# Performance work log

Hardware: AMD Instinct MI355X
Metric: run time of the kernel (lower is better)

Reference implementation:

```python
import jax, jax.numpy as jnp
import numpy as np

IMG_SIZES = [56, 28, 14, 7]


def setup_inputs() -> dict:
    key = jax.random.key(0)
    k0, k1, k2, k3, kp = jax.random.split(key, 5)
    return {
        "feat0": jax.random.normal(k0, (8, 64, 56, 56), dtype=jnp.float32),
        "feat1": jax.random.normal(k1, (8, 128, 28, 28), dtype=jnp.float32),
        "feat2": jax.random.normal(k2, (8, 256, 14, 14), dtype=jnp.float32),
        "feat3": jax.random.normal(k3, (8, 512, 7, 7), dtype=jnp.float32),
        "pts": jax.random.normal(kp, (131072, 3), dtype=jnp.float32),
        "batch": 3,
    }


def _project(feat, h, w, size):
    # feat: [C, size, size]; h, w: [N] float in [0, 223]
    x = h / (224.0 / size)
    y = w / (224.0 / size)
    x1 = jnp.floor(x).astype(jnp.int32)
    x2 = jnp.minimum(jnp.ceil(x).astype(jnp.int32), size - 1)
    y1 = jnp.floor(y).astype(jnp.int32)
    y2 = jnp.minimum(jnp.ceil(y).astype(jnp.int32), size - 1)
    # NOTE: original casts x,y to long BEFORE computing weights (truncation),
    # so weights are integer 0/1 -- reproduced faithfully.
    xl = x.astype(jnp.int32)
    yl = y.astype(jnp.int32)
    g = lambda xi, yi: feat[:, xi, yi].T  # [N, C] gather
    w11 = ((x2 - xl) * (y2 - yl)).astype(feat.dtype)[:, None]
    w12 = ((x2 - xl) * (yl - y1)).astype(feat.dtype)[:, None]
    w21 = ((xl - x1) * (y2 - yl)).astype(feat.dtype)[:, None]
    w22 = ((xl - x1) * (yl - y1)).astype(feat.dtype)[:, None]
    return w11 * g(x1, y1) + w21 * g(x2, y1) + w12 * g(x1, y2) + w22 * g(x2, y2)


def reference(feat0, feat1, feat2, feat3, pts, batch):
    h = 248.0 * (pts[:, 1] / pts[:, 2]) + 111.5
    w = 248.0 * (pts[:, 0] / (-pts[:, 2])) + 111.5
    h = jnp.clip(h, 0.0, 223.0)
    w = jnp.clip(w, 0.0, 223.0)
    feats = [feat0[batch], feat1[batch], feat2[batch], feat3[batch]]
    outs = [_project(f, h, w, s) for f, s in zip(feats, IMG_SIZES)]
    return jnp.concatenate(outs, axis=1)  # [N, 960]
```

## Files before the change

### kernel.cpp

```cpp
#include <hip/hip_runtime.h>
#include <hip/hip_bf16.h>

#define NPTS 131072
#define FT_TOTAL 376320

typedef float f32x4 __attribute__((ext_vector_type(4)));

__global__ __launch_bounds__(256) void k_indices(
    const float* __restrict__ pts,
    int4* __restrict__ idx4)
{
    int n = blockIdx.x * 256 + threadIdx.x;
    if (n >= NPTS) return;
    float px = pts[3 * n + 0];
    float py = pts[3 * n + 1];
    float pz = pts[3 * n + 2];
    float qh = __fdiv_rn(py, pz);
    float qw = __fdiv_rn(px, -pz);
    float h = __fadd_rn(__fmul_rn(248.0f, qh), 111.5f);
    float w = __fadd_rn(__fmul_rn(248.0f, qw), 111.5f);
    h = fminf(fmaxf(h, 0.0f), 223.0f);
    w = fminf(fmaxf(w, 0.0f), 223.0f);

    const float scl[4] = {0.25f, 0.125f, 0.0625f, 0.03125f};
    const int   S[4]   = {56, 28, 14, 7};
    int r[4];
#pragma unroll
    for (int s = 0; s < 4; ++s) {
        float x = h * scl[s];
        float y = w * scl[s];
        int x1 = (int)floorf(x);
        int x2 = min((int)ceilf(x), S[s] - 1);
        int y1 = (int)floorf(y);
        int y2 = min((int)ceilf(y), S[s] - 1);
        int bit = (x2 - x1) * (y2 - y1);
        r[s] = bit ? (x1 * S[s] + y1) : -1;
    }
    idx4[n] = make_int4(r[0], r[1], r[2], r[3]);
}

__global__ __launch_bounds__(256) void k_transpose(
    const float* __restrict__ f0,
    const float* __restrict__ f1,
    const float* __restrict__ f2,
    const float* __restrict__ f3,
    const int* __restrict__ batch,
    float* __restrict__ ft)
{
    int d = blockIdx.x * 256 + threadIdx.x;
    if (d >= FT_TOTAL) return;
    int b = *batch;
    const float* src;
    int local, c, p, hw;
    if (d < 200704) {
        local = d;          c = local & 63;  p = local >> 6; hw = 3136;
        src = f0 + (size_t)b * 64 * 3136;
    } else if (d < 301056) {
        local = d - 200704; c = local & 127; p = local >> 7; hw = 784;
        src = f1 + (size_t)b * 128 * 784;
    } else if (d < 351232) {
        local = d - 301056; c = local & 255; p = local >> 8; hw = 196;
        src = f2 + (size_t)b * 256 * 196;
    } else {
        local = d - 351232; c = local & 511; p = local >> 9; hw = 49;
        src = f3 + (size_t)b * 512 * 49;
    }
    ft[d] = src[c * hw + p];
}

__global__ __launch_bounds__(256) void k_gather(
    const int* __restrict__ idx,
    const float* __restrict__ ft,
    float* __restrict__ out)
{
    int gid = blockIdx.x * 256 + threadIdx.x;
    int n = gid / 240;
    int j = gid - n * 240;

    int s, C, toff, cb;
    if (j < 16)       { s = 0; C = 64;  toff = 0;      cb = j * 4; }
    else if (j < 48)  { s = 1; C = 128; toff = 200704; cb = (j - 16) * 4; }
    else if (j < 112) { s = 2; C = 256; toff = 301056; cb = (j - 48) * 4; }
    else              { s = 3; C = 512; toff = 351232; cb = (j - 112) * 4; }

    int id = idx[n * 4 + s];
    f32x4 v = (f32x4)(0.0f);
    if (id >= 0) {
        v = *(const f32x4*)(ft + toff + id * C + cb);
    }
    f32x4* dst = (f32x4*)(out + (size_t)n * 960 + j * 4);
    __builtin_nontemporal_store(v, dst);
}

extern "C" void kernel_launch(void* const* d_in, const int* in_sizes, int n_in,
                              void* d_out, int out_size, void* d_ws, size_t ws_size,
                              hipStream_t stream) {
    const float* f0  = (const float*)d_in[0];
    const float* f1  = (const float*)d_in[1];
    const float* f2  = (const float*)d_in[2];
    const float* f3  = (const float*)d_in[3];
    const float* pts = (const float*)d_in[4];
    const int* batch = (const int*)d_in[5];

    int4* idx4 = (int4*)d_ws;
    float* ft = (float*)((char*)d_ws + (size_t)NPTS * 16);
    float* out = (float*)d_out;

    k_indices<<<NPTS / 256, 256, 0, stream>>>(pts, idx4);
    k_transpose<<<(FT_TOTAL + 255) / 256, 256, 0, stream>>>(f0, f1, f2, f3, batch, ft);
    k_gather<<<122880, 256, 0, stream>>>((const int*)idx4, ft, out);
}
```

Baseline: 485.9 us.

## Fuse index and transpose kernels; gather one point per wavefront

Merges the index-computation and feature-transpose kernels into one launch that splits work by block range, removing a kernel launch and its serialization. The gather kernel now gives each 64-lane wavefront one point: it loads the four indices once as an int4 and loops over the 240 float4 output chunks, instead of doing a per-thread divide by 240 and a scalar index load. Some lanes are idle in the last loop iteration (240 of 256 slots used), and each thread carries more work.

```diff
diff --git a/kernel.cpp b/kernel.cpp
--- a/kernel.cpp
+++ b/kernel.cpp
@@ -1,45 +1,13 @@
 #include <hip/hip_runtime.h>
-#include <hip/hip_bf16.h>
 
 #define NPTS 131072
 #define FT_TOTAL 376320
 
 typedef float f32x4 __attribute__((ext_vector_type(4)));
 
-__global__ __launch_bounds__(256) void k_indices(
+__global__ __launch_bounds__(256) void k_prep(
     const float* __restrict__ pts,
-    int4* __restrict__ idx4)
-{
-    int n = blockIdx.x * 256 + threadIdx.x;
-    if (n >= NPTS) return;
-    float px = pts[3 * n + 0];
-    float py = pts[3 * n + 1];
-    float pz = pts[3 * n + 2];
-    float qh = __fdiv_rn(py, pz);
-    float qw = __fdiv_rn(px, -pz);
-    float h = __fadd_rn(__fmul_rn(248.0f, qh), 111.5f);
-    float w = __fadd_rn(__fmul_rn(248.0f, qw), 111.5f);
-    h = fminf(fmaxf(h, 0.0f), 223.0f);
-    w = fminf(fmaxf(w, 0.0f), 223.0f);
-
-    const float scl[4] = {0.25f, 0.125f, 0.0625f, 0.03125f};
-    const int   S[4]   = {56, 28, 14, 7};
-    int r[4];
-#pragma unroll
-    for (int s = 0; s < 4; ++s) {
-        float x = h * scl[s];
-        float y = w * scl[s];
-        int x1 = (int)floorf(x);
-        int x2 = min((int)ceilf(x), S[s] - 1);
-        int y1 = (int)floorf(y);
-        int y2 = min((int)ceilf(y), S[s] - 1);
-        int bit = (x2 - x1) * (y2 - y1);
-        r[s] = bit ? (x1 * S[s] + y1) : -1;
-    }
-    idx4[n] = make_int4(r[0], r[1], r[2], r[3]);
-}
-
-__global__ __launch_bounds__(256) void k_transpose(
+    int4* __restrict__ idx4,
     const float* __restrict__ f0,
     const float* __restrict__ f1,
     const float* __restrict__ f2,
@@ -47,25 +15,54 @@
     const int* __restrict__ batch,
     float* __restrict__ ft)
 {
-    int d = blockIdx.x * 256 + threadIdx.x;
-    if (d >= FT_TOTAL) return;
-    int b = *batch;
-    const float* src;
-    int local, c, p, hw;
-    if (d < 200704) {
-        local = d;          c = local & 63;  p = local >> 6; hw = 3136;
-        src = f0 + (size_t)b * 64 * 3136;
-    } else if (d < 301056) {
-        local = d - 200704; c = local & 127; p = local >> 7; hw = 784;
-        src = f1 + (size_t)b * 128 * 784;
-    } else if (d < 351232) {
-        local = d - 301056; c = local & 255; p = local >> 8; hw = 196;
-        src = f2 + (size_t)b * 256 * 196;
+    int blk = blockIdx.x;
+    if (blk < 512) {
+        int n = blk * 256 + threadIdx.x;
+        float px = pts[3 * n + 0];
+        float py = pts[3 * n + 1];
+        float pz = pts[3 * n + 2];
+        float qh = __fdiv_rn(py, pz);
+        float qw = __fdiv_rn(px, -pz);
+        float h = __fadd_rn(__fmul_rn(248.0f, qh), 111.5f);
+        float w = __fadd_rn(__fmul_rn(248.0f, qw), 111.5f);
+        h = fminf(fmaxf(h, 0.0f), 223.0f);
+        w = fminf(fmaxf(w, 0.0f), 223.0f);
+
+        const float scl[4] = {0.25f, 0.125f, 0.0625f, 0.03125f};
+        const int   S[4]   = {56, 28, 14, 7};
+        int r[4];
+#pragma unroll
+        for (int s = 0; s < 4; ++s) {
+            float x = h * scl[s];
+            float y = w * scl[s];
+            int x1 = (int)floorf(x);
+            int x2 = min((int)ceilf(x), S[s] - 1);
+            int y1 = (int)floorf(y);
+            int y2 = min((int)ceilf(y), S[s] - 1);
+            int bit = (x2 - x1) * (y2 - y1);
+            r[s] = bit ? (x1 * S[s] + y1) : -1;
+        }
+        idx4[n] = make_int4(r[0], r[1], r[2], r[3]);
     } else {
-        local = d - 351232; c = local & 511; p = local >> 9; hw = 49;
-        src = f3 + (size_t)b * 512 * 49;
+        int d = (blk - 512) * 256 + threadIdx.x;
+        int b = *batch;
+        const float* src;
+        int local, c, p, hw;
+        if (d < 200704) {
+            local = d;          c = local & 63;  p = local >> 6; hw = 3136;
+            src = f0 + (size_t)b * 64 * 3136;
+        } else if (d < 301056) {
+            local = d - 200704; c = local & 127; p = local >> 7; hw = 784;
+            src = f1 + (size_t)b * 128 * 784;
+        } else if (d < 351232) {
+            local = d - 301056; c = local & 255; p = local >> 8; hw = 196;
+            src = f2 + (size_t)b * 256 * 196;
+        } else {
+            local = d - 351232; c = local & 511; p = local >> 9; hw = 49;
+            src = f3 + (size_t)b * 512 * 49;
+        }
+        ft[d] = src[c * hw + p];
     }
-    ft[d] = src[c * hw + p];
 }
 
 __global__ __launch_bounds__(256) void k_gather(
@@ -73,23 +70,28 @@
     const float* __restrict__ ft,
     float* __restrict__ out)
 {
-    int gid = blockIdx.x * 256 + threadIdx.x;
-    int n = gid / 240;
-    int j = gid - n * 240;
+    const int lane = threadIdx.x & 63;
+    const int n = blockIdx.x * 4 + (threadIdx.x >> 6);
+    const int4 ids = *(const int4*)(idx + n * 4);
+    float* dst = out + (size_t)n * 960;
 
-    int s, C, toff, cb;
-    if (j < 16)       { s = 0; C = 64;  toff = 0;      cb = j * 4; }
-    else if (j < 48)  { s = 1; C = 128; toff = 200704; cb = (j - 16) * 4; }
-    else if (j < 112) { s = 2; C = 256; toff = 301056; cb = (j - 48) * 4; }
-    else              { s = 3; C = 512; toff = 351232; cb = (j - 112) * 4; }
-
-    int id = idx[n * 4 + s];
-    f32x4 v = (f32x4)(0.0f);
-    if (id >= 0) {
-        v = *(const f32x4*)(ft + toff + id * C + cb);
+#pragma unroll
+    for (int k = 0; k < 4; ++k) {
+        int j = lane + k * 64;
+        if (j < 240) {
+            int s  = (j >= 16) + (j >= 48) + (j >= 112);
+            int id = (s == 0) ? ids.x : (s == 1) ? ids.y
+                   : (s == 2) ? ids.z : ids.w;
+            int C    = 64 << s;
+            int toff = (s == 0) ? 0      : (s == 1) ? 200704
+                     : (s == 2) ? 301056 : 351232;
+            int jb   = (s == 0) ? 0 : (s == 1) ? 16 : (s == 2) ? 48 : 112;
+            f32x4 v = (f32x4)(0.0f);
+            if (id >= 0)
+                v = *(const f32x4*)(ft + toff + id * C + (j - jb) * 4);
+            __builtin_nontemporal_store(v, (f32x4*)(dst + j * 4));
+        }
     }
-    f32x4* dst = (f32x4*)(out + (size_t)n * 960 + j * 4);
-    __builtin_nontemporal_store(v, dst);
 }
 
 extern "C" void kernel_launch(void* const* d_in, const int* in_sizes, int n_in,
@@ -106,7 +108,6 @@
     float* ft = (float*)((char*)d_ws + (size_t)NPTS * 16);
     float* out = (float*)d_out;
 
-    k_indices<<<NPTS / 256, 256, 0, stream>>>(pts, idx4);
-    k_transpose<<<(FT_TOTAL + 255) / 256, 256, 0, stream>>>(f0, f1, f2, f3, batch, ft);
-    k_gather<<<122880, 256, 0, stream>>>((const int*)idx4, ft, out);
+    k_prep<<<512 + 1470, 256, 0, stream>>>(pts, idx4, f0, f1, f2, f3, batch, ft);
+    k_gather<<<NPTS / 4, 256, 0, stream>>>((const int*)idx4, ft, out);
 }
```

Measured after the change: 502.7 us. +3.4%, slower.
